# Performance work log

Hardware: AMD Instinct MI355X
Metric: run time of the kernel (lower is better)

## Reference

```python
import jax, jax.numpy as jnp
import numpy as np

T, B, D_IN, D_H, D_MID, D_OUT = 16, 16384, 64, 256, 64, 4


def setup_inputs() -> dict:
    key = jax.random.key(0)
    ks = jax.random.split(key, 12)
    s = 0.05
    return {
        "x": jax.random.normal(ks[0], (T, B, D_IN), dtype=jnp.float32),
        "hc1": jnp.zeros((B, D_H), dtype=jnp.float32),
        "W_i2h": jax.random.normal(ks[1], (D_H, D_IN), dtype=jnp.float32) * s,
        "b_i2h": jax.random.normal(ks[2], (D_H,), dtype=jnp.float32) * s,
        "W_h2h": jax.random.normal(ks[3], (D_H, D_H), dtype=jnp.float32) * s,
        "b_h2h": jax.random.normal(ks[4], (D_H,), dtype=jnp.float32) * s,
        "W_h2o": jax.random.normal(ks[5], (D_MID, D_H), dtype=jnp.float32) * s,
        "b_h2o": jax.random.normal(ks[6], (D_MID,), dtype=jnp.float32) * s,
        "W_fc": jax.random.normal(ks[7], (D_OUT, D_MID), dtype=jnp.float32) * s,
        "b_fc": jax.random.normal(ks[8], (D_OUT,), dtype=jnp.float32) * s,
    }


def reference(x, hc1, W_i2h, b_i2h, W_h2h, b_h2h, W_h2o, b_h2o, W_fc, b_fc):
    # 16-step vanilla RNN: h = tanh(i2h(x_t) + h2h(h)); out = fc(tanh(h2o(h)))
    def step(h, xt):
        h_new = jnp.tanh(xt @ W_i2h.T + b_i2h + h @ W_h2h.T + b_h2h)  # [B, 256]
        out = jnp.tanh(h_new @ W_h2o.T + b_h2o) @ W_fc.T + b_fc       # [B, 4]
        return h_new, out

    h_final, output_seq = jax.lax.scan(step, hc1, x)
    return output_seq, h_final
```

## Files before the change

### kernel.cpp

```cpp
#include <hip/hip_runtime.h>


typedef _Float16 half8 __attribute__((ext_vector_type(8)));
typedef float floatx4 __attribute__((ext_vector_type(4)));

#define T_STEPS  16
#define BATCH    16384
#define BLK_ROWS 32
#define HS       264
#define MS       72

__device__ inline float fast_tanh(float x) {
    float t = __builtin_amdgcn_exp2f(x * 2.8853900817779268f);
    return 1.0f - 2.0f * __builtin_amdgcn_rcpf(t + 1.0f);
}

__device__ inline half8 cvt8(const float* __restrict__ p) {
    float4 a = ((const float4*)p)[0];
    float4 b = ((const float4*)p)[1];
    half8 h;
    h[0] = (_Float16)a.x; h[1] = (_Float16)a.y; h[2] = (_Float16)a.z; h[3] = (_Float16)a.w;
    h[4] = (_Float16)b.x; h[5] = (_Float16)b.y; h[6] = (_Float16)b.z; h[7] = (_Float16)b.w;
    return h;
}

__global__ __launch_bounds__(256, 2) void rnn_kernel(
    const float* __restrict__ x,   const float* __restrict__ hc1,
    const float* __restrict__ Wi,  const float* __restrict__ bi,
    const float* __restrict__ Wh,  const float* __restrict__ bh,
    const float* __restrict__ Wo,  const float* __restrict__ bo,
    const float* __restrict__ Wf,  const float* __restrict__ bf,
    float* __restrict__ out)
{
    __shared__ _Float16 h_lds[BLK_ROWS * HS];
    __shared__ _Float16 mid_lds[BLK_ROWS * MS];
    __shared__ float    biasPre[256];
    __shared__ float    bo_lds[64];
    __shared__ _Float16 wfc_lds[4 * 64];
    __shared__ float    bfc_lds[4];

    const int tid  = threadIdx.x;
    const int w    = tid >> 6;
    const int lane = tid & 63;
    const int l16  = lane & 15;
    const int quad = lane >> 4;
    const int b0   = blockIdx.x * BLK_ROWS;

    biasPre[tid] = bi[tid] + bh[tid];
    if (tid < 64) bo_lds[tid] = bo[tid];
    wfc_lds[tid] = (_Float16)Wf[tid];
    if (tid < 4) bfc_lds[tid] = bf[tid];

    {
        int r = tid >> 3, c0 = (tid & 7) * 32;
        const float4* src = (const float4*)&hc1[(size_t)(b0 + r) * 256 + c0];
        #pragma unroll
        for (int i = 0; i < 8; ++i) {
            float4 v = src[i];
            int c = c0 + i * 4;
            h_lds[r * HS + c + 0] = (_Float16)v.x;
            h_lds[r * HS + c + 1] = (_Float16)v.y;
            h_lds[r * HS + c + 2] = (_Float16)v.z;
            h_lds[r * HS + c + 3] = (_Float16)v.w;
        }
    }

    half8 wcat[10][4];
    #pragma unroll
    for (int ks = 0; ks < 10; ++ks) {
        #pragma unroll
        for (int nt = 0; nt < 4; ++nt) {
            int j = w * 64 + nt * 16 + l16;
            const float* src = (ks < 2)
                ? (Wi + (size_t)j * 64  + ks * 32 + quad * 8)
                : (Wh + (size_t)j * 256 + (ks - 2) * 32 + quad * 8);
            wcat[ks][nt] = cvt8(src);
        }
    }
    half8 wof[8];
    #pragma unroll
    for (int ks = 0; ks < 8; ++ks) {
        int j = w * 16 + l16;
        wof[ks] = cvt8(Wo + (size_t)j * 256 + ks * 32 + quad * 8);
    }

    __syncthreads();

    for (int t = 0; t < T_STEPS; ++t) {
        half8 afx[2][2];
        #pragma unroll
        for (int mt = 0; mt < 2; ++mt) {
            int m = mt * 16 + l16;
            const float* xr = x + ((size_t)t * BATCH + b0 + m) * 64;
            #pragma unroll
            for (int k2 = 0; k2 < 2; ++k2)
                afx[mt][k2] = cvt8(xr + k2 * 32 + quad * 8);
        }

        floatx4 acc[2][4];
        #pragma unroll
        for (int mt = 0; mt < 2; ++mt)
            #pragma unroll
            for (int nt = 0; nt < 4; ++nt)
                acc[mt][nt] = (floatx4){0.f, 0.f, 0.f, 0.f};

        #pragma unroll
        for (int ks = 0; ks < 10; ++ks) {
            half8 af[2];
            #pragma unroll
            for (int mt = 0; mt < 2; ++mt) {
                if (ks < 2) {
                    af[mt] = afx[mt][ks];
                } else {
                    int m = mt * 16 + l16;
                    af[mt] = *(const half8*)&h_lds[m * HS + (ks - 2) * 32 + quad * 8];
                }
            }
            #pragma unroll
            for (int mt = 0; mt < 2; ++mt)
                #pragma unroll
                for (int nt = 0; nt < 4; ++nt)
                    acc[mt][nt] = __builtin_amdgcn_mfma_f32_16x16x32_f16(
                        af[mt], wcat[ks][nt], acc[mt][nt], 0, 0, 0);
        }

        __syncthreads();

        #pragma unroll
        for (int nt = 0; nt < 4; ++nt) {
            int col = w * 64 + nt * 16 + l16;
            float bias = biasPre[col];
            #pragma unroll
            for (int mt = 0; mt < 2; ++mt) {
                #pragma unroll
                for (int r = 0; r < 4; ++r) {
                    int row = mt * 16 + quad * 4 + r;
                    h_lds[row * HS + col] = (_Float16)fast_tanh(acc[mt][nt][r] + bias);
                }
            }
        }

        __syncthreads();

        floatx4 acc2[2];
        #pragma unroll
        for (int mt = 0; mt < 2; ++mt) acc2[mt] = (floatx4){0.f, 0.f, 0.f, 0.f};
        #pragma unroll
        for (int ks = 0; ks < 8; ++ks) {
            #pragma unroll
            for (int mt = 0; mt < 2; ++mt) {
                int m = mt * 16 + l16;
                half8 af = *(const half8*)&h_lds[m * HS + ks * 32 + quad * 8];
                acc2[mt] = __builtin_amdgcn_mfma_f32_16x16x32_f16(
                    af, wof[ks], acc2[mt], 0, 0, 0);
            }
        }
        {
            int col = w * 16 + l16;
            float bias = bo_lds[col];
            #pragma unroll
            for (int mt = 0; mt < 2; ++mt)
                #pragma unroll
                for (int r = 0; r < 4; ++r) {
                    int row = mt * 16 + quad * 4 + r;
                    mid_lds[row * MS + col] = (_Float16)fast_tanh(acc2[mt][r] + bias);
                }
        }

        __syncthreads();

        if (tid < 128) {
            int row = tid >> 2, oc = tid & 3;
            float s = bfc_lds[oc];
            #pragma unroll
            for (int k8 = 0; k8 < 64; k8 += 8) {
                half8 mv = *(const half8*)&mid_lds[row * MS + k8];
                half8 wv = *(const half8*)&wfc_lds[oc * 64 + k8];
                #pragma unroll
                for (int j = 0; j < 8; ++j)
                    s += (float)mv[j] * (float)wv[j];
            }
            out[((size_t)t * BATCH + b0 + row) * 4 + oc] = s;
        }
    }

    {
        int r = tid >> 3, c0 = (tid & 7) * 32;
        float4* dst = (float4*)&out[(size_t)T_STEPS * BATCH * 4 + (size_t)(b0 + r) * 256 + c0];
        #pragma unroll
        for (int i = 0; i < 8; ++i) {
            int c = c0 + i * 4;
            float4 v;
            v.x = (float)h_lds[r * HS + c + 0];
            v.y = (float)h_lds[r * HS + c + 1];
            v.z = (float)h_lds[r * HS + c + 2];
            v.w = (float)h_lds[r * HS + c + 3];
            dst[i] = v;
        }
    }
}

extern "C" void kernel_launch(void* const* d_in, const int* in_sizes, int n_in,
                              void* d_out, int out_size, void* d_ws, size_t ws_size,
                              hipStream_t stream) {
    const float* x   = (const float*)d_in[0];
    const float* hc1 = (const float*)d_in[1];
    const float* Wi  = (const float*)d_in[2];
    const float* bi  = (const float*)d_in[3];
    const float* Wh  = (const float*)d_in[4];
    const float* bh  = (const float*)d_in[5];
    const float* Wo  = (const float*)d_in[6];
    const float* bo  = (const float*)d_in[7];
    const float* Wf  = (const float*)d_in[8];
    const float* bf  = (const float*)d_in[9];

    rnn_kernel<<<BATCH / BLK_ROWS, 256, 0, stream>>>(
        x, hc1, Wi, bi, Wh, bh, Wo, bo, Wf, bf, (float*)d_out);
}
```

Baseline: 221.3 us.

## Split RNN block across eight waves with double-buffered hidden state and x prefetch

Doubles threads per block to 512 so each wave computes 32 hidden columns instead of 64, which halves the weight registers per thread. The hidden state is double-buffered in LDS, removing one barrier per step, and x for the next step is prefetched into registers. A separate prep kernel converts the weights to fp16 once in workspace. The trade-offs are an extra kernel launch and idle waves during the h2o and fc stages.

```diff
diff --git a/kernel.cpp b/kernel.cpp
--- a/kernel.cpp
+++ b/kernel.cpp
@@ -10,34 +10,47 @@
 #define HS       264
 #define MS       72
 
+#define WS_WI 0
+#define WS_WH 16384
+#define WS_WO 81920
+#define WS_WF 98304
+#define WS_TOT 98560
+
+__global__ void prep_kernel(const float* __restrict__ Wi, const float* __restrict__ Wh,
+                            const float* __restrict__ Wo, const float* __restrict__ Wf,
+                            _Float16* __restrict__ ws) {
+    int i = blockIdx.x * 256 + threadIdx.x;
+    if (i >= WS_TOT) return;
+    float v;
+    if (i < WS_WH)      v = Wi[i];
+    else if (i < WS_WO) v = Wh[i - WS_WH];
+    else if (i < WS_WF) v = Wo[i - WS_WO];
+    else                v = Wf[i - WS_WF];
+    ws[i] = (_Float16)v;
+}
+
 __device__ inline float fast_tanh(float x) {
     float t = __builtin_amdgcn_exp2f(x * 2.8853900817779268f);
     return 1.0f - 2.0f * __builtin_amdgcn_rcpf(t + 1.0f);
 }
 
-__device__ inline half8 cvt8(const float* __restrict__ p) {
-    float4 a = ((const float4*)p)[0];
-    float4 b = ((const float4*)p)[1];
+__device__ inline half8 cvt8pair(float4 a, float4 b) {
     half8 h;
     h[0] = (_Float16)a.x; h[1] = (_Float16)a.y; h[2] = (_Float16)a.z; h[3] = (_Float16)a.w;
     h[4] = (_Float16)b.x; h[5] = (_Float16)b.y; h[6] = (_Float16)b.z; h[7] = (_Float16)b.w;
     return h;
 }
 
-__global__ __launch_bounds__(256, 2) void rnn_kernel(
-    const float* __restrict__ x,   const float* __restrict__ hc1,
-    const float* __restrict__ Wi,  const float* __restrict__ bi,
-    const float* __restrict__ Wh,  const float* __restrict__ bh,
-    const float* __restrict__ Wo,  const float* __restrict__ bo,
-    const float* __restrict__ Wf,  const float* __restrict__ bf,
+__global__ __launch_bounds__(512, 4) void rnn_kernel(
+    const float* __restrict__ x,    const float* __restrict__ hc1,
+    const _Float16* __restrict__ wf16,
+    const float* __restrict__ bi,   const float* __restrict__ bh,
+    const float* __restrict__ bo,   const float* __restrict__ bfc,
     float* __restrict__ out)
 {
-    __shared__ _Float16 h_lds[BLK_ROWS * HS];
+    __shared__ _Float16 h_lds[2][BLK_ROWS * HS];
     __shared__ _Float16 mid_lds[BLK_ROWS * MS];
-    __shared__ float    biasPre[256];
-    __shared__ float    bo_lds[64];
-    __shared__ _Float16 wfc_lds[4 * 64];
-    __shared__ float    bfc_lds[4];
+    __shared__ _Float16 wfc_lds[256];
 
     const int tid  = threadIdx.x;
     const int w    = tid >> 6;
@@ -45,133 +58,147 @@
     const int l16  = lane & 15;
     const int quad = lane >> 4;
     const int b0   = blockIdx.x * BLK_ROWS;
-
-    biasPre[tid] = bi[tid] + bh[tid];
-    if (tid < 64) bo_lds[tid] = bo[tid];
-    wfc_lds[tid] = (_Float16)Wf[tid];
-    if (tid < 4) bfc_lds[tid] = bf[tid];
-
-    {
-        int r = tid >> 3, c0 = (tid & 7) * 32;
-        const float4* src = (const float4*)&hc1[(size_t)(b0 + r) * 256 + c0];
-        #pragma unroll
-        for (int i = 0; i < 8; ++i) {
-            float4 v = src[i];
-            int c = c0 + i * 4;
-            h_lds[r * HS + c + 0] = (_Float16)v.x;
-            h_lds[r * HS + c + 1] = (_Float16)v.y;
-            h_lds[r * HS + c + 2] = (_Float16)v.z;
-            h_lds[r * HS + c + 3] = (_Float16)v.w;
-        }
-    }
-
-    half8 wcat[10][4];
+    const int cb   = w * 32;
+
+    if (tid < 256) wfc_lds[tid] = wf16[WS_WF + tid];
+
+    float bpre[2];
+    #pragma unroll
+    for (int nt = 0; nt < 2; ++nt) {
+        int c = cb + nt * 16 + l16;
+        bpre[nt] = bi[c] + bh[c];
+    }
+    float bo_r  = (w < 4) ? bo[w * 16 + l16] : 0.0f;
+    float bfc_r = (tid >= 256 && tid < 384) ? bfc[(tid - 256) & 3] : 0.0f;
+
+    half8 wcat[10][2];
     #pragma unroll
     for (int ks = 0; ks < 10; ++ks) {
         #pragma unroll
-        for (int nt = 0; nt < 4; ++nt) {
-            int j = w * 64 + nt * 16 + l16;
-            const float* src = (ks < 2)
-                ? (Wi + (size_t)j * 64  + ks * 32 + quad * 8)
-                : (Wh + (size_t)j * 256 + (ks - 2) * 32 + quad * 8);
-            wcat[ks][nt] = cvt8(src);
+        for (int nt = 0; nt < 2; ++nt) {
+            int j = cb + nt * 16 + l16;
+            wcat[ks][nt] = (ks < 2)
+                ? *(const half8*)(wf16 + WS_WI + (size_t)j * 64  + ks * 32 + quad * 8)
+                : *(const half8*)(wf16 + WS_WH + (size_t)j * 256 + (ks - 2) * 32 + quad * 8);
         }
     }
     half8 wof[8];
+    if (w < 4) {
+        #pragma unroll
+        for (int ks = 0; ks < 8; ++ks)
+            wof[ks] = *(const half8*)(wf16 + WS_WO + (size_t)(w * 16 + l16) * 256 + ks * 32 + quad * 8);
+    }
+
+    {
+        int r = tid >> 4, c0 = (tid & 15) * 16;
+        const float4* src = (const float4*)&hc1[(size_t)(b0 + r) * 256 + c0];
+        float4 v0 = src[0], v1 = src[1], v2 = src[2], v3 = src[3];
+        *(half8*)&h_lds[0][r * HS + c0]     = cvt8pair(v0, v1);
+        *(half8*)&h_lds[0][r * HS + c0 + 8] = cvt8pair(v2, v3);
+    }
+
+    float4 xraw[2][4];
     #pragma unroll
-    for (int ks = 0; ks < 8; ++ks) {
-        int j = w * 16 + l16;
-        wof[ks] = cvt8(Wo + (size_t)j * 256 + ks * 32 + quad * 8);
+    for (int mt = 0; mt < 2; ++mt) {
+        const float* base = x + (size_t)(b0 + mt * 16 + l16) * 64 + quad * 8;
+        xraw[mt][0] = ((const float4*)base)[0];
+        xraw[mt][1] = ((const float4*)base)[1];
+        xraw[mt][2] = ((const float4*)(base + 32))[0];
+        xraw[mt][3] = ((const float4*)(base + 32))[1];
     }
 
     __syncthreads();
 
     for (int t = 0; t < T_STEPS; ++t) {
+        const int cur = t & 1, nxt = cur ^ 1;
+
         half8 afx[2][2];
         #pragma unroll
         for (int mt = 0; mt < 2; ++mt) {
-            int m = mt * 16 + l16;
-            const float* xr = x + ((size_t)t * BATCH + b0 + m) * 64;
-            #pragma unroll
-            for (int k2 = 0; k2 < 2; ++k2)
-                afx[mt][k2] = cvt8(xr + k2 * 32 + quad * 8);
-        }
-
-        floatx4 acc[2][4];
+            afx[mt][0] = cvt8pair(xraw[mt][0], xraw[mt][1]);
+            afx[mt][1] = cvt8pair(xraw[mt][2], xraw[mt][3]);
+        }
+        if (t + 1 < T_STEPS) {
+            #pragma unroll
+            for (int mt = 0; mt < 2; ++mt) {
+                const float* base = x + ((size_t)(t + 1) * BATCH + b0 + mt * 16 + l16) * 64 + quad * 8;
+                xraw[mt][0] = ((const float4*)base)[0];
+                xraw[mt][1] = ((const float4*)base)[1];
+                xraw[mt][2] = ((const float4*)(base + 32))[0];
+                xraw[mt][3] = ((const float4*)(base + 32))[1];
+            }
+        }
+
+        floatx4 acc[2][2];
         #pragma unroll
         for (int mt = 0; mt < 2; ++mt)
             #pragma unroll
-            for (int nt = 0; nt < 4; ++nt)
+            for (int nt = 0; nt < 2; ++nt)
                 acc[mt][nt] = (floatx4){0.f, 0.f, 0.f, 0.f};
 
         #pragma unroll
-        for (int ks = 0; ks < 10; ++ks) {
+        for (int ks = 2; ks < 10; ++ks) {
             half8 af[2];
             #pragma unroll
-            for (int mt = 0; mt < 2; ++mt) {
-                if (ks < 2) {
-                    af[mt] = afx[mt][ks];
-                } else {
-                    int m = mt * 16 + l16;
-                    af[mt] = *(const half8*)&h_lds[m * HS + (ks - 2) * 32 + quad * 8];
+            for (int mt = 0; mt < 2; ++mt)
+                af[mt] = *(const half8*)&h_lds[cur][(mt * 16 + l16) * HS + (ks - 2) * 32 + quad * 8];
+            #pragma unroll
+            for (int mt = 0; mt < 2; ++mt)
+                #pragma unroll
+                for (int nt = 0; nt < 2; ++nt)
+                    acc[mt][nt] = __builtin_amdgcn_mfma_f32_16x16x32_f16(
+                        af[mt], wcat[ks][nt], acc[mt][nt], 0, 0, 0);
+        }
+        #pragma unroll
+        for (int ks = 0; ks < 2; ++ks)
+            #pragma unroll
+            for (int mt = 0; mt < 2; ++mt)
+                #pragma unroll
+                for (int nt = 0; nt < 2; ++nt)
+                    acc[mt][nt] = __builtin_amdgcn_mfma_f32_16x16x32_f16(
+                        afx[mt][ks], wcat[ks][nt], acc[mt][nt], 0, 0, 0);
+
+        #pragma unroll
+        for (int nt = 0; nt < 2; ++nt) {
+            int col = cb + nt * 16 + l16;
+            #pragma unroll
+            for (int mt = 0; mt < 2; ++mt)
+                #pragma unroll
+                for (int r = 0; r < 4; ++r) {
+                    int row = mt * 16 + quad * 4 + r;
+                    h_lds[nxt][row * HS + col] = (_Float16)fast_tanh(acc[mt][nt][r] + bpre[nt]);
+                }
+        }
+
+        __syncthreads();
+
+        if (w < 4) {
+            floatx4 acc2[2];
+            #pragma unroll
+            for (int mt = 0; mt < 2; ++mt) acc2[mt] = (floatx4){0.f, 0.f, 0.f, 0.f};
+            #pragma unroll
+            for (int ks = 0; ks < 8; ++ks) {
+                #pragma unroll
+                for (int mt = 0; mt < 2; ++mt) {
+                    half8 af = *(const half8*)&h_lds[nxt][(mt * 16 + l16) * HS + ks * 32 + quad * 8];
+                    acc2[mt] = __builtin_amdgcn_mfma_f32_16x16x32_f16(af, wof[ks], acc2[mt], 0, 0, 0);
                 }
             }
-            #pragma unroll
-            for (int mt = 0; mt < 2; ++mt)
-                #pragma unroll
-                for (int nt = 0; nt < 4; ++nt)
-                    acc[mt][nt] = __builtin_amdgcn_mfma_f32_16x16x32_f16(
-                        af[mt], wcat[ks][nt], acc[mt][nt], 0, 0, 0);
-        }
-
-        __syncthreads();
-
-        #pragma unroll
-        for (int nt = 0; nt < 4; ++nt) {
-            int col = w * 64 + nt * 16 + l16;
-            float bias = biasPre[col];
-            #pragma unroll
-            for (int mt = 0; mt < 2; ++mt) {
+            int col = w * 16 + l16;
+            #pragma unroll
+            for (int mt = 0; mt < 2; ++mt)
                 #pragma unroll
                 for (int r = 0; r < 4; ++r) {
                     int row = mt * 16 + quad * 4 + r;
-                    h_lds[row * HS + col] = (_Float16)fast_tanh(acc[mt][nt][r] + bias);
+                    mid_lds[row * MS + col] = (_Float16)fast_tanh(acc2[mt][r] + bo_r);
                 }
-            }
         }
 
         __syncthreads();
 
-        floatx4 acc2[2];
-        #pragma unroll
-        for (int mt = 0; mt < 2; ++mt) acc2[mt] = (floatx4){0.f, 0.f, 0.f, 0.f};
-        #pragma unroll
-        for (int ks = 0; ks < 8; ++ks) {
-            #pragma unroll
-            for (int mt = 0; mt < 2; ++mt) {
-                int m = mt * 16 + l16;
-                half8 af = *(const half8*)&h_lds[m * HS + ks * 32 + quad * 8];
-                acc2[mt] = __builtin_amdgcn_mfma_f32_16x16x32_f16(
-                    af, wof[ks], acc2[mt], 0, 0, 0);
-            }
-        }
-        {
-            int col = w * 16 + l16;
-            float bias = bo_lds[col];
-            #pragma unroll
-            for (int mt = 0; mt < 2; ++mt)
-                #pragma unroll
-                for (int r = 0; r < 4; ++r) {
-                    int row = mt * 16 + quad * 4 + r;
-                    mid_lds[row * MS + col] = (_Float16)fast_tanh(acc2[mt][r] + bias);
-                }
-        }
-
-        __syncthreads();
-
-        if (tid < 128) {
-            int row = tid >> 2, oc = tid & 3;
-            float s = bfc_lds[oc];
+        if (tid >= 256 && tid < 384) {
+            int idx = tid - 256, row = idx >> 2, oc = idx & 3;
+            float s = bfc_r;
             #pragma unroll
             for (int k8 = 0; k8 < 64; k8 += 8) {
                 half8 mv = *(const half8*)&mid_lds[row * MS + k8];
@@ -185,18 +212,15 @@
     }
 
     {
-        int r = tid >> 3, c0 = (tid & 7) * 32;
+        int r = tid >> 4, c0 = (tid & 15) * 16;
         float4* dst = (float4*)&out[(size_t)T_STEPS * BATCH * 4 + (size_t)(b0 + r) * 256 + c0];
-        #pragma unroll
-        for (int i = 0; i < 8; ++i) {
-            int c = c0 + i * 4;
-            float4 v;
-            v.x = (float)h_lds[r * HS + c + 0];
-            v.y = (float)h_lds[r * HS + c + 1];
-            v.z = (float)h_lds[r * HS + c + 2];
-            v.w = (float)h_lds[r * HS + c + 3];
-            dst[i] = v;
-        }
+        half8 p0 = *(const half8*)&h_lds[0][r * HS + c0];
+        half8 p1 = *(const half8*)&h_lds[0][r * HS + c0 + 8];
+        float4 v;
+        v.x = (float)p0[0]; v.y = (float)p0[1]; v.z = (float)p0[2]; v.w = (float)p0[3]; dst[0] = v;
+        v.x = (float)p0[4]; v.y = (float)p0[5]; v.z = (float)p0[6]; v.w = (float)p0[7]; dst[1] = v;
+        v.x = (float)p1[0]; v.y = (float)p1[1]; v.z = (float)p1[2]; v.w = (float)p1[3]; dst[2] = v;
+        v.x = (float)p1[4]; v.y = (float)p1[5]; v.z = (float)p1[6]; v.w = (float)p1[7]; dst[3] = v;
     }
 }
 
@@ -213,7 +237,9 @@
     const float* bo  = (const float*)d_in[7];
     const float* Wf  = (const float*)d_in[8];
     const float* bf  = (const float*)d_in[9];
-
-    rnn_kernel<<<BATCH / BLK_ROWS, 256, 0, stream>>>(
-        x, hc1, Wi, bi, Wh, bh, Wo, bo, Wf, bf, (float*)d_out);
-}
+    _Float16* ws = (_Float16*)d_ws;
+
+    prep_kernel<<<(WS_TOT + 255) / 256, 256, 0, stream>>>(Wi, Wh, Wo, Wf, ws);
+    rnn_kernel<<<BATCH / BLK_ROWS, 512, 0, stream>>>(
+        x, hc1, ws, bi, bh, bo, bf, (float*)d_out);
+}
```

Result: slower. 352.0 us (+59.0%).
